# Kernel tuning notes

Measured on AMD Instinct MI355X. Metric: run time of the kernel, lower is better.

The kernel has to match this reference:

```python
import jax, jax.numpy as jnp
import numpy as np

B, S, D, U = 8, 2048, 256, 128


def setup_inputs() -> dict:
    key = jax.random.key(0)
    ks = jax.random.split(key, 5)
    inputs = jax.random.normal(ks[0], (B, S, D), dtype=jnp.float32)
    W_q = jax.random.normal(ks[1], (D, U), dtype=jnp.float32) * (1.0 / np.sqrt(D))
    W_k = jax.random.normal(ks[2], (D, U), dtype=jnp.float32) * (1.0 / np.sqrt(D))
    W_v = jax.random.normal(ks[3], (D, U), dtype=jnp.float32) * (1.0 / np.sqrt(D))
    W_o = jax.random.normal(ks[4], (U, D), dtype=jnp.float32) * (1.0 / np.sqrt(U))
    b_o = jnp.zeros((D,), dtype=jnp.float32)
    return {"inputs": inputs, "W_q": W_q, "W_k": W_k, "W_v": W_v, "W_o": W_o, "b_o": b_o}


def reference(inputs, W_q, W_k, W_v, W_o, b_o):
    # QKV projections: [B,S,D] @ [D,U] -> [B,S,U]
    Q = jnp.einsum('bsd,du->bsu', inputs, W_q)
    K = jnp.einsum('bsd,du->bsu', inputs, W_k)
    V = jnp.einsum('bsd,du->bsu', inputs, W_v)
    scale = 1.0 / jnp.sqrt(jnp.asarray(U, dtype=inputs.dtype))
    # scores: [B,S,S]
    attn = jnp.einsum('bqu,bku->bqk', Q, K) * scale
    w = jax.nn.softmax(attn, axis=-1)
    out = jnp.einsum('bqk,bku->bqu', w, V)  # [B,S,U]
    # output projection + residual
    return jnp.einsum('bsu,ud->bsd', out, W_o) + b_o + inputs
```

## Files before the change

kernel.cpp:

```cpp
#include <hip/hip_runtime.h>
#include <hip/hip_bf16.h>

#define B_ 8
#define S_ 2048
#define D_ 256
#define U_ 128
#define BS_ (B_*S_)

using bf16 = __hip_bfloat16;
typedef __attribute__((ext_vector_type(8))) __bf16 bf8v;
typedef __attribute__((ext_vector_type(4))) float f4v;
typedef __attribute__((ext_vector_type(16))) float f16v;
typedef __attribute__((ext_vector_type(4))) float float4v;
typedef __attribute__((ext_vector_type(4))) unsigned short us4;
typedef __attribute__((ext_vector_type(8))) unsigned short us8;
typedef __attribute__((ext_vector_type(4))) unsigned int u4v;
typedef __attribute__((ext_vector_type(2))) unsigned int u2v;

#define MFMA16(a,b,c) __builtin_amdgcn_mfma_f32_16x16x32_bf16((a),(b),(c),0,0,0)
#define MFMA32(a,b,c) __builtin_amdgcn_mfma_f32_32x32x16_bf16((a),(b),(c),0,0,0)

#if __has_builtin(__builtin_amdgcn_exp2f)
#define EXP2(x) __builtin_amdgcn_exp2f(x)
#else
#define EXP2(x) exp2f(x)
#endif

__device__ __forceinline__ unsigned short f2bits(float f){
  return __builtin_bit_cast(unsigned short, __float2bfloat16(f));
}
__device__ __forceinline__ float b2f(unsigned short u){
  return __builtin_bit_cast(float, ((unsigned)u) << 16);
}

__device__ __forceinline__ void plswap(unsigned &a, unsigned &b){
#if __has_builtin(__builtin_amdgcn_permlane32_swap)
  u2v r = __builtin_amdgcn_permlane32_swap(a, b, 0, 0);
  a = r[0]; b = r[1];
#else
  unsigned as = (unsigned)__shfl_xor((int)a, 32);
  unsigned bs = (unsigned)__shfl_xor((int)b, 32);
  bool hi = (threadIdx.x & 32) != 0;
  unsigned na = hi ? bs : a;
  unsigned nb = hi ? b  : as;
  a = na; b = nb;
#endif
}
__device__ __forceinline__ float cross_max(float x){
  unsigned a = __builtin_bit_cast(unsigned, x), b = a;
  plswap(a, b);
  return fmaxf(__builtin_bit_cast(float, a), __builtin_bit_cast(float, b));
}
__device__ __forceinline__ float cross_sum(float x){
  unsigned a = __builtin_bit_cast(unsigned, x), b = a;
  plswap(a, b);
  return __builtin_bit_cast(float, a) + __builtin_bit_cast(float, b);
}

__device__ __forceinline__ void gload16(const void* g, void* l){
  __builtin_amdgcn_global_load_lds(
    (const __attribute__((address_space(1))) char*)(unsigned long long)g,
    (__attribute__((address_space(3))) char*)(unsigned int)(unsigned long long)l,
    16, 0, 0);
}

__global__ __launch_bounds__(256) void prep_w_kernel(const float* __restrict__ Wq,
                                                     const float* __restrict__ Wk,
                                                     const float* __restrict__ Wv,
                                                     const float* __restrict__ Wo,
                                                     bf16* __restrict__ Wqf,
                                                     bf16* __restrict__ Wkf,
                                                     bf16* __restrict__ Wvf,
                                                     bf16* __restrict__ Wof){
  int t = blockIdx.x*256 + threadIdx.x;
  int which = t >> 12;
  int c = t & 4095;
  int lane = c & 63;
  int lq = lane & 15, g = lane >> 4;
  us8 v;
  if (which < 3){
    int nt = c >> 9;
    int ks = (c >> 6) & 7;
    const float* src = (which==0)?Wq:((which==1)?Wk:Wv);
    bf16* dst = (which==0)?Wqf:((which==1)?Wkf:Wvf);
    #pragma unroll
    for (int j=0;j<8;j++) v[j] = f2bits(src[(size_t)(ks*32 + g*8 + j)*U_ + nt*16 + lq]);
    *reinterpret_cast<us8*>(dst + (size_t)c*8) = v;
  } else {
    int nt = c >> 8;
    int ks = (c >> 6) & 3;
    #pragma unroll
    for (int j=0;j<8;j++) v[j] = f2bits(Wo[(size_t)(ks*32 + g*8 + j)*D_ + nt*16 + lq]);
    *reinterpret_cast<us8*>(Wof + (size_t)c*8) = v;
  }
}

__global__ __launch_bounds__(256) void qkv_kernel(const float* __restrict__ X,
                                                  const bf16* __restrict__ Wqf,
                                                  const bf16* __restrict__ Wkf,
                                                  const bf16* __restrict__ Wvf,
                                                  bf16* __restrict__ Q,
                                                  bf16* __restrict__ K,
                                                  bf16* __restrict__ Vt){
  __shared__ unsigned short Xls[32][264];

  const int tid  = threadIdx.x;
  const int w    = tid >> 6;
  const int lane = tid & 63;
  const int lq   = lane & 15;
  const int g    = lane >> 4;
  const int m0   = blockIdx.x*32;
  const int n0   = w*32;

  #pragma unroll
  for (int p=0; p<8; p++){
    int row = p*4 + (tid>>6);
    int col = (tid & 63)*4;
    float4v x = *reinterpret_cast<const float4v*>(X + (size_t)(m0+row)*D_ + col);
    us4 v;
    #pragma unroll
    for (int j=0;j<4;j++) v[j] = f2bits(x[j]);
    *reinterpret_cast<us4*>(&Xls[row][col]) = v;
  }
  __syncthreads();

  bf8v af[2][8];
  #pragma unroll
  for (int rt=0; rt<2; rt++)
    #pragma unroll
    for (int ks=0; ks<8; ks++)
      af[rt][ks] = *reinterpret_cast<const bf8v*>(&Xls[rt*16+lq][ks*32 + g*8]);

  #pragma unroll
  for (int which=0; which<3; which++){
    const bf16* Wf = (which==0) ? Wqf : ((which==1) ? Wkf : Wvf);
    f4v acc[2][2];
    #pragma unroll
    for (int rt=0;rt<2;rt++)
      #pragma unroll
      for (int ct=0;ct<2;ct++) acc[rt][ct] = (f4v){0.f,0.f,0.f,0.f};

    #pragma unroll
    for (int ks=0; ks<8; ks++){
      #pragma unroll
      for (int ct=0; ct<2; ct++){
        int nt = (n0>>4) + ct;
        bf8v b = *reinterpret_cast<const bf8v*>(Wf + ((size_t)((nt*8 + ks)*64 + lane) << 3));
        acc[0][ct] = MFMA16(af[0][ks], b, acc[0][ct]);
        acc[1][ct] = MFMA16(af[1][ks], b, acc[1][ct]);
      }
    }

    if (which==0){
      const float qscale = 0.12751745562008530f;
      #pragma unroll
      for (int rt=0;rt<2;rt++)
        #pragma unroll
        for (int ct=0;ct<2;ct++)
          #pragma unroll
          for (int r=0;r<4;r++)
            Q[(size_t)(m0+rt*16+g*4+r)*U_ + n0+ct*16+lq] = __float2bfloat16(acc[rt][ct][r]*qscale);
    } else if (which==1){
      #pragma unroll
      for (int rt=0;rt<2;rt++)
        #pragma unroll
        for (int ct=0;ct<2;ct++)
          #pragma unroll
          for (int r=0;r<4;r++)
            K[(size_t)(m0+rt*16+g*4+r)*U_ + n0+ct*16+lq] = __float2bfloat16(acc[rt][ct][r]);
    } else {
      #pragma unroll
      for (int rt=0;rt<2;rt++)
        #pragma unroll
        for (int ct=0;ct<2;ct++)
          #pragma unroll
          for (int r=0;r<4;r++){
            int m = m0 + rt*16 + g*4 + r;
            int bb = m >> 11;
            int ss = m & (S_-1);
            Vt[((size_t)bb*U_ + n0+ct*16+lq)*S_ + ss] = __float2bfloat16(acc[rt][ct][r]);
          }
    }
  }
}

__global__ __launch_bounds__(256) void flash_kernel(const bf16* __restrict__ Q,
                                                    const bf16* __restrict__ K,
                                                    const bf16* __restrict__ Vt,
                                                    bf16* __restrict__ Opart,
                                                    float* __restrict__ Mst,
                                                    float* __restrict__ Lst,
                                                    int nsplit){
  __shared__ bf16 Kls[2][64*128];
  __shared__ bf16 Vls[2][128*64];

  const int n    = blockIdx.x;
  const int b    = n & 7;
  const int m    = n >> 3;
  const int s    = m % nsplit;
  const int qt   = m / nsplit;
  const int w    = threadIdx.x >> 6;
  const int lane = threadIdx.x & 63;
  const int l5   = lane & 31;
  const int hi   = lane >> 5;
  const int q0   = qt*128 + w*32;

  const int NT = S_/64;
  const int t0 = (s*NT)/nsplit;
  const int t1 = ((s+1)*NT)/nsplit;

  const bf16* Qp = Q + (size_t)(b*S_ + q0 + l5)*U_ + hi*8;
  bf8v qf[8];
  #pragma unroll
  for (int uc=0; uc<8; uc++) qf[uc] = *reinterpret_cast<const bf8v*>(Qp + uc*16);

  f16v o[4];
  #pragma unroll
  for (int uc=0; uc<4; uc++)
    #pragma unroll
    for (int r=0; r<16; r++) o[uc][r] = 0.f;

  float mrow = -1e30f, lrow = 0.f;

  const bf16* Kbase = K  + (size_t)b*S_*U_;
  const bf16* Vtb   = Vt + (size_t)b*U_*S_;

  auto stageK = [&](int buf, int t){
    const int r0 = w*16;
    #pragma unroll
    for (int c=0; c<4; c++){
      int row  = r0 + c*4 + (lane>>4);
      int soff = ((lane&15)<<4) ^ ((row&7)<<4);
      const char* src = (const char*)(Kbase + (size_t)(t*64 + row)*U_) + soff;
      gload16(src, (void*)&Kls[buf][(r0 + c*4)*128]);
    }
  };
  auto stageV = [&](int buf, int t){
    const int r0 = w*32;
    #pragma unroll
    for (int c=0; c<4; c++){
      int u    = r0 + c*8 + (lane>>3);
      int soff = ((lane&7)<<4) ^ ((u&7)<<4);
      const char* src = (const char*)(Vtb + (size_t)u*S_ + t*64) + soff;
      gload16(src, (void*)&Vls[buf][(r0 + c*8)*64]);
    }
  };

  auto process = [&](f16v &st, const char* vb0, int sub){
    float p[16];
    #pragma unroll
    for (int r=0;r<16;r++) p[r] = st[r];

    float a0 = fmaxf(p[0],p[1]),  a1 = fmaxf(p[2],p[3]);
    float a2 = fmaxf(p[4],p[5]),  a3 = fmaxf(p[6],p[7]);
    float a4 = fmaxf(p[8],p[9]),  a5 = fmaxf(p[10],p[11]);
    float a6 = fmaxf(p[12],p[13]),a7 = fmaxf(p[14],p[15]);
    float b0 = fmaxf(a0,a1), b1 = fmaxf(a2,a3), b2 = fmaxf(a4,a5), b3 = fmaxf(a6,a7);
    float tm = fmaxf(fmaxf(b0,b1), fmaxf(b2,b3));
    tm = cross_max(tm);

    if (!__all(tm <= mrow + 11.54f)){
      float mn    = fmaxf(mrow, tm);
      float alpha = EXP2(mrow - mn);
      lrow *= alpha;
      #pragma unroll
      for (int uc=0;uc<4;uc++)
        #pragma unroll
        for (int r=0;r<16;r++) o[uc][r] *= alpha;
      mrow = mn;
    }

    #pragma unroll
    for (int r=0;r<16;r++) p[r] = EXP2(p[r]-mrow);
    float s0s = (p[0]+p[1]) + (p[2]+p[3]);
    float s1s = (p[4]+p[5]) + (p[6]+p[7]);
    float s2s = (p[8]+p[9]) + (p[10]+p[11]);
    float s3s = (p[12]+p[13]) + (p[14]+p[15]);
    lrow += cross_sum((s0s+s1s) + (s2s+s3s));

    unsigned c0 = (unsigned)f2bits(p[0])  | ((unsigned)f2bits(p[1])<<16);
    unsigned c1 = (unsigned)f2bits(p[2])  | ((unsigned)f2bits(p[3])<<16);
    unsigned c2 = (unsigned)f2bits(p[4])  | ((unsigned)f2bits(p[5])<<16);
    unsigned c3 = (unsigned)f2bits(p[6])  | ((unsigned)f2bits(p[7])<<16);
    unsigned c4 = (unsigned)f2bits(p[8])  | ((unsigned)f2bits(p[9])<<16);
    unsigned c5 = (unsigned)f2bits(p[10]) | ((unsigned)f2bits(p[11])<<16);
    unsigned c6 = (unsigned)f2bits(p[12]) | ((unsigned)f2bits(p[13])<<16);
    unsigned c7 = (unsigned)f2bits(p[14]) | ((unsigned)f2bits(p[15])<<16);
    plswap(c0, c2);
    plswap(c1, c3);
    plswap(c4, c6);
    plswap(c5, c7);
    u4v w0v = {c0, c1, c2, c3};
    u4v w1v = {c4, c5, c6, c7};
    bf8v pa0 = __builtin_bit_cast(bf8v, w0v);
    bf8v pa1 = __builtin_bit_cast(bf8v, w1v);

    __builtin_amdgcn_s_setprio(1);
    #pragma unroll
    for (int uc=0; uc<4; uc++){
      const char* vrow = vb0 + (uc*32 + l5)*128;
      bf8v v0 = *reinterpret_cast<const bf8v*>(vrow + ((sub*64      + hi*16) ^ ((l5&7)<<4)));
      bf8v v1 = *reinterpret_cast<const bf8v*>(vrow + ((sub*64 + 32 + hi*16) ^ ((l5&7)<<4)));
      o[uc] = MFMA32(v0, pa0, o[uc]);
      o[uc] = MFMA32(v1, pa1, o[uc]);
    }
    __builtin_amdgcn_s_setprio(0);
  };

  stageK(0, t0); stageV(0, t0);
  int cur = 0;
  for (int tt=t0; tt<t1; ++tt){
    int tn = (tt+1 < NT) ? (tt+1) : (NT-1);
    stageK(cur^1, tn); stageV(cur^1, tn);
    asm volatile("s_waitcnt vmcnt(8)" ::: "memory");
    __builtin_amdgcn_s_barrier();
    unsigned bufoff = (unsigned)cur * 16384u;
    asm volatile("" : "+v"(bufoff) : : "memory");
    const char* kb0 = (const char*)&Kls[0][0] + bufoff;
    const char* vb0 = (const char*)&Vls[0][0] + bufoff;

    f16v stA, stB;
    #pragma unroll
    for (int r=0;r<16;r++){ stA[r]=0.f; stB[r]=0.f; }
    __builtin_amdgcn_s_setprio(1);
    #pragma unroll
    for (int uc=0; uc<4; uc++){
      bf8v ka = *reinterpret_cast<const bf8v*>(kb0 + l5*256 + ((uc*64      + hi*16) ^ ((l5&7)<<4)));
      bf8v kc = *reinterpret_cast<const bf8v*>(kb0 + l5*256 + ((uc*64 + 32 + hi*16) ^ ((l5&7)<<4)));
      stA = MFMA32(ka, qf[2*uc],   stA);
      stA = MFMA32(kc, qf[2*uc+1], stA);
    }
    #pragma unroll
    for (int uc=0; uc<4; uc++){
      bf8v ka = *reinterpret_cast<const bf8v*>(kb0 + 8192 + l5*256 + ((uc*64      + hi*16) ^ ((l5&7)<<4)));
      bf8v kc = *reinterpret_cast<const bf8v*>(kb0 + 8192 + l5*256 + ((uc*64 + 32 + hi*16) ^ ((l5&7)<<4)));
      stB = MFMA32(ka, qf[2*uc],   stB);
      stB = MFMA32(kc, qf[2*uc+1], stB);
    }
    __builtin_amdgcn_s_setprio(0);

    process(stA, vb0, 0);
    process(stB, vb0, 1);

    asm volatile("" ::: "memory");
    __builtin_amdgcn_s_barrier();
    cur ^= 1;
  }

  const size_t rowg = (size_t)(b*S_ + q0 + l5);
  if (hi==0){
    Mst[(size_t)s*BS_ + rowg] = mrow;
    Lst[(size_t)s*BS_ + rowg] = lrow;
  }
  float inv = 1.0f / lrow;
  bf16* Op = Opart + (size_t)s*BS_*U_ + rowg*U_;
  #pragma unroll
  for (int uc=0; uc<4; uc++){
    #pragma unroll
    for (int g2=0; g2<4; g2++){
      us4 outv;
      #pragma unroll
      for (int j=0;j<4;j++) outv[j] = f2bits(o[uc][g2*4+j]*inv);
      *reinterpret_cast<us4*>(Op + uc*32 + g2*8 + hi*4) = outv;
    }
  }
}

template<int NS>
__global__ __launch_bounds__(256) void oproj_kernel(const bf16* __restrict__ Opart,
                                                    const float* __restrict__ Mst,
                                                    const float* __restrict__ Lst,
                                                    const bf16* __restrict__ Wof,
                                                    const float* __restrict__ X,
                                                    const float* __restrict__ bo,
                                                    float* __restrict__ Y){
  __shared__ unsigned short Als[64][136];

  const int tid  = threadIdx.x;
  const int w    = tid >> 6;
  const int lane = tid & 63;
  const int lq   = lane & 15;
  const int g    = lane >> 4;
  const int m0   = blockIdx.x*64;
  const int n0   = blockIdx.y*128;

  const unsigned short* Ou = reinterpret_cast<const unsigned short*>(Opart);
  #pragma unroll
  for (int p=0; p<4; p++){
    int rl  = p*16 + (tid>>4);
    int c8  = (tid & 15)*8;
    int row = m0 + rl;
    float cw[NS];
    float M = -1e30f;
    #pragma unroll
    for (int s=0;s<NS;s++){ cw[s] = Mst[(size_t)s*BS_ + row]; M = fmaxf(M, cw[s]); }
    float L = 0.f;
    #pragma unroll
    for (int s=0;s<NS;s++){ cw[s] = Lst[(size_t)s*BS_ + row]*EXP2(cw[s]-M); L += cw[s]; }
    float inv = 1.0f / L;
    float av[8];
    #pragma unroll
    for (int j=0;j<8;j++) av[j] = 0.f;
    #pragma unroll
    for (int s=0;s<NS;s++){
      us8 pp = *reinterpret_cast<const us8*>(Ou + (size_t)s*BS_*U_ + (size_t)row*U_ + c8);
      #pragma unroll
      for (int j=0;j<8;j++) av[j] += cw[s]*b2f(pp[j]);
    }
    us8 aw;
    #pragma unroll
    for (int j=0;j<8;j++) aw[j] = f2bits(av[j]*inv);
    *reinterpret_cast<us8*>(&Als[rl][c8]) = aw;
  }
  __syncthreads();

  f4v acc[8];
  #pragma unroll
  for (int i=0;i<8;i++) acc[i] = (f4v){0.f,0.f,0.f,0.f};

  #pragma unroll
  for (int ks=0; ks<4; ks++){
    bf8v a = *reinterpret_cast<const bf8v*>(&Als[w*16+lq][ks*32 + g*8]);
    #pragma unroll
    for (int nc=0;nc<8;nc++){
      int nt = (n0>>4) + nc;
      bf8v bb = *reinterpret_cast<const bf8v*>(Wof + ((size_t)((nt*4 + ks)*64 + lane) << 3));
      acc[nc] = MFMA16(a, bb, acc[nc]);
    }
  }

  #pragma unroll
  for (int nc=0;nc<8;nc++){
    int col = n0 + nc*16 + lq;
    float bias = bo[col];
    #pragma unroll
    for (int r=0;r<4;r++){
      int orow = m0 + w*16 + g*4 + r;
      Y[(size_t)orow*D_ + col] = acc[nc][r] + bias + X[(size_t)orow*D_ + col];
    }
  }
}

extern "C" void kernel_launch(void* const* d_in, const int* in_sizes, int n_in,
                              void* d_out, int out_size, void* d_ws, size_t ws_size,
                              hipStream_t stream) {
  (void)in_sizes; (void)n_in; (void)out_size;
  const float* X  = (const float*)d_in[0];
  const float* Wq = (const float*)d_in[1];
  const float* Wk = (const float*)d_in[2];
  const float* Wv = (const float*)d_in[3];
  const float* Wo = (const float*)d_in[4];
  const float* bo = (const float*)d_in[5];
  float* Y = (float*)d_out;

  const size_t MB = 1u<<20;
  int nsplit = (ws_size >= 30408704u) ? 4 : 2;

  char* ws = (char*)d_ws;
  bf16* Opart = (bf16*)ws;
  size_t off = (size_t)nsplit*4*MB;
  bf16* Qb  = (bf16*)(ws + off); off += 4*MB;
  bf16* Kb  = (bf16*)(ws + off); off += 4*MB;
  bf16* Vtb = (bf16*)(ws + off); off += 4*MB;
  bf16* Wqf = (bf16*)(ws + off); off += 65536;
  bf16* Wkf = (bf16*)(ws + off); off += 65536;
  bf16* Wvf = (bf16*)(ws + off); off += 65536;
  bf16* Wof = (bf16*)(ws + off); off += 65536;
  float* Mst = (float*)(ws + off); off += (size_t)nsplit*BS_*4;
  float* Lst = (float*)(ws + off);

  prep_w_kernel<<<dim3(64), dim3(256), 0, stream>>>(Wq, Wk, Wv, Wo, Wqf, Wkf, Wvf, Wof);
  qkv_kernel<<<dim3(BS_/32), dim3(256), 0, stream>>>(X, Wqf, Wkf, Wvf, Qb, Kb, Vtb);
  flash_kernel<<<dim3(16*nsplit*8), dim3(256), 0, stream>>>(Qb, Kb, Vtb, Opart, Mst, Lst, nsplit);
  if (nsplit == 4){
    oproj_kernel<4><<<dim3(BS_/64, 2), dim3(256), 0, stream>>>(Opart, Mst, Lst, Wof, X, bo, Y);
  } else {
    oproj_kernel<2><<<dim3(BS_/64, 2), dim3(256), 0, stream>>>(Opart, Mst, Lst, Wof, X, bo, Y);
  }
}
```

Before: 69.29 us.

## Halve flash KV tile to 32 keys, raise occupancy, allow 8-way split-K

The flash kernel now processes 32-key tiles instead of 64-key tiles. This halves LDS per block, drops the second score accumulator, and uses a new V swizzle for the narrower rows. Launch bounds now request 4 blocks per CU, and an 8-way KV split is used when the workspace is large enough, giving more blocks to fill the GPU. The cost is more loop iterations with barriers per key, and more partial outputs for the output-projection kernel to merge.

```diff
diff --git a/kernel.cpp b/kernel.cpp
--- a/kernel.cpp
+++ b/kernel.cpp
@@ -184,15 +184,15 @@
   }
 }
 
-__global__ __launch_bounds__(256) void flash_kernel(const bf16* __restrict__ Q,
-                                                    const bf16* __restrict__ K,
-                                                    const bf16* __restrict__ Vt,
-                                                    bf16* __restrict__ Opart,
-                                                    float* __restrict__ Mst,
-                                                    float* __restrict__ Lst,
-                                                    int nsplit){
-  __shared__ bf16 Kls[2][64*128];
-  __shared__ bf16 Vls[2][128*64];
+__global__ __launch_bounds__(256, 4) void flash_kernel(const bf16* __restrict__ Q,
+                                                       const bf16* __restrict__ K,
+                                                       const bf16* __restrict__ Vt,
+                                                       bf16* __restrict__ Opart,
+                                                       float* __restrict__ Mst,
+                                                       float* __restrict__ Lst,
+                                                       int nsplit){
+  __shared__ bf16 Kls[2][32*128];
+  __shared__ bf16 Vls[2][128*32];
 
   const int n    = blockIdx.x;
   const int b    = n & 7;
@@ -205,7 +205,7 @@
   const int hi   = lane >> 5;
   const int q0   = qt*128 + w*32;
 
-  const int NT = S_/64;
+  const int NT = S_/32;
   const int t0 = (s*NT)/nsplit;
   const int t1 = ((s+1)*NT)/nsplit;
 
@@ -226,31 +226,54 @@
   const bf16* Vtb   = Vt + (size_t)b*U_*S_;
 
   auto stageK = [&](int buf, int t){
-    const int r0 = w*16;
-    #pragma unroll
-    for (int c=0; c<4; c++){
+    const int r0 = w*8;
+    #pragma unroll
+    for (int c=0; c<2; c++){
       int row  = r0 + c*4 + (lane>>4);
       int soff = ((lane&15)<<4) ^ ((row&7)<<4);
-      const char* src = (const char*)(Kbase + (size_t)(t*64 + row)*U_) + soff;
+      const char* src = (const char*)(Kbase + (size_t)(t*32 + row)*U_) + soff;
       gload16(src, (void*)&Kls[buf][(r0 + c*4)*128]);
     }
   };
   auto stageV = [&](int buf, int t){
     const int r0 = w*32;
     #pragma unroll
-    for (int c=0; c<4; c++){
-      int u    = r0 + c*8 + (lane>>3);
-      int soff = ((lane&7)<<4) ^ ((u&7)<<4);
-      const char* src = (const char*)(Vtb + (size_t)u*S_ + t*64) + soff;
-      gload16(src, (void*)&Vls[buf][(r0 + c*8)*64]);
+    for (int c=0; c<2; c++){
+      int u    = r0 + c*16 + (lane>>2);
+      int soff = (((lane&3) ^ ((u>>1)&3)) << 4);
+      const char* src = (const char*)(Vtb + (size_t)u*S_ + t*32) + soff;
+      gload16(src, (void*)&Vls[buf][(r0 + c*16)*32]);
     }
   };
 
-  auto process = [&](f16v &st, const char* vb0, int sub){
+  stageK(0, t0); stageV(0, t0);
+  int cur = 0;
+  for (int tt=t0; tt<t1; ++tt){
+    int tn = (tt+1 < NT) ? (tt+1) : (NT-1);
+    stageK(cur^1, tn); stageV(cur^1, tn);
+    asm volatile("s_waitcnt vmcnt(4)" ::: "memory");
+    __builtin_amdgcn_s_barrier();
+    unsigned bufoff = (unsigned)cur * 8192u;
+    asm volatile("" : "+v"(bufoff) : : "memory");
+    const char* kb = (const char*)&Kls[0][0] + bufoff;
+    const char* vb = (const char*)&Vls[0][0] + bufoff;
+
+    f16v st;
+    #pragma unroll
+    for (int r=0;r<16;r++) st[r] = 0.f;
+    __builtin_amdgcn_s_setprio(1);
+    #pragma unroll
+    for (int uc=0; uc<4; uc++){
+      bf8v ka = *reinterpret_cast<const bf8v*>(kb + l5*256 + ((uc*64      + hi*16) ^ ((l5&7)<<4)));
+      bf8v kc = *reinterpret_cast<const bf8v*>(kb + l5*256 + ((uc*64 + 32 + hi*16) ^ ((l5&7)<<4)));
+      st = MFMA32(ka, qf[2*uc],   st);
+      st = MFMA32(kc, qf[2*uc+1], st);
+    }
+    __builtin_amdgcn_s_setprio(0);
+
     float p[16];
     #pragma unroll
     for (int r=0;r<16;r++) p[r] = st[r];
-
     float a0 = fmaxf(p[0],p[1]),  a1 = fmaxf(p[2],p[3]);
     float a2 = fmaxf(p[4],p[5]),  a3 = fmaxf(p[6],p[7]);
     float a4 = fmaxf(p[8],p[9]),  a5 = fmaxf(p[10],p[11]);
@@ -298,49 +321,15 @@
     __builtin_amdgcn_s_setprio(1);
     #pragma unroll
     for (int uc=0; uc<4; uc++){
-      const char* vrow = vb0 + (uc*32 + l5)*128;
-      bf8v v0 = *reinterpret_cast<const bf8v*>(vrow + ((sub*64      + hi*16) ^ ((l5&7)<<4)));
-      bf8v v1 = *reinterpret_cast<const bf8v*>(vrow + ((sub*64 + 32 + hi*16) ^ ((l5&7)<<4)));
+      int u = uc*32 + l5;
+      const char* vrow = vb + u*64;
+      int swz = ((u>>1)&3) << 4;
+      bf8v v0 = *reinterpret_cast<const bf8v*>(vrow + ((hi*16)      ^ swz));
+      bf8v v1 = *reinterpret_cast<const bf8v*>(vrow + ((32 + hi*16) ^ swz));
       o[uc] = MFMA32(v0, pa0, o[uc]);
       o[uc] = MFMA32(v1, pa1, o[uc]);
     }
     __builtin_amdgcn_s_setprio(0);
-  };
-
-  stageK(0, t0); stageV(0, t0);
-  int cur = 0;
-  for (int tt=t0; tt<t1; ++tt){
-    int tn = (tt+1 < NT) ? (tt+1) : (NT-1);
-    stageK(cur^1, tn); stageV(cur^1, tn);
-    asm volatile("s_waitcnt vmcnt(8)" ::: "memory");
-    __builtin_amdgcn_s_barrier();
-    unsigned bufoff = (unsigned)cur * 16384u;
-    asm volatile("" : "+v"(bufoff) : : "memory");
-    const char* kb0 = (const char*)&Kls[0][0] + bufoff;
-    const char* vb0 = (const char*)&Vls[0][0] + bufoff;
-
-    f16v stA, stB;
-    #pragma unroll
-    for (int r=0;r<16;r++){ stA[r]=0.f; stB[r]=0.f; }
-    __builtin_amdgcn_s_setprio(1);
-    #pragma unroll
-    for (int uc=0; uc<4; uc++){
-      bf8v ka = *reinterpret_cast<const bf8v*>(kb0 + l5*256 + ((uc*64      + hi*16) ^ ((l5&7)<<4)));
-      bf8v kc = *reinterpret_cast<const bf8v*>(kb0 + l5*256 + ((uc*64 + 32 + hi*16) ^ ((l5&7)<<4)));
-      stA = MFMA32(ka, qf[2*uc],   stA);
-      stA = MFMA32(kc, qf[2*uc+1], stA);
-    }
-    #pragma unroll
-    for (int uc=0; uc<4; uc++){
-      bf8v ka = *reinterpret_cast<const bf8v*>(kb0 + 8192 + l5*256 + ((uc*64      + hi*16) ^ ((l5&7)<<4)));
-      bf8v kc = *reinterpret_cast<const bf8v*>(kb0 + 8192 + l5*256 + ((uc*64 + 32 + hi*16) ^ ((l5&7)<<4)));
-      stB = MFMA32(ka, qf[2*uc],   stB);
-      stB = MFMA32(kc, qf[2*uc+1], stB);
-    }
-    __builtin_amdgcn_s_setprio(0);
-
-    process(stA, vb0, 0);
-    process(stB, vb0, 1);
 
     asm volatile("" ::: "memory");
     __builtin_amdgcn_s_barrier();
@@ -454,7 +443,7 @@
   float* Y = (float*)d_out;
 
   const size_t MB = 1u<<20;
-  int nsplit = (ws_size >= 30408704u) ? 4 : 2;
+  int nsplit = (ws_size >= 47448064u) ? 8 : ((ws_size >= 30408704u) ? 4 : 2);
 
   char* ws = (char*)d_ws;
   bf16* Opart = (bf16*)ws;
@@ -472,7 +461,9 @@
   prep_w_kernel<<<dim3(64), dim3(256), 0, stream>>>(Wq, Wk, Wv, Wo, Wqf, Wkf, Wvf, Wof);
   qkv_kernel<<<dim3(BS_/32), dim3(256), 0, stream>>>(X, Wqf, Wkf, Wvf, Qb, Kb, Vtb);
   flash_kernel<<<dim3(16*nsplit*8), dim3(256), 0, stream>>>(Qb, Kb, Vtb, Opart, Mst, Lst, nsplit);
-  if (nsplit == 4){
+  if (nsplit == 8){
+    oproj_kernel<8><<<dim3(BS_/64, 2), dim3(256), 0, stream>>>(Opart, Mst, Lst, Wof, X, bo, Y);
+  } else if (nsplit == 4){
     oproj_kernel<4><<<dim3(BS_/64, 2), dim3(256), 0, stream>>>(Opart, Mst, Lst, Wof, X, bo, Y);
   } else {
     oproj_kernel<2><<<dim3(BS_/64, 2), dim3(256), 0, stream>>>(Opart, Mst, Lst, Wof, X, bo, Y);
```

After: 91.89 us. 1.33x slower.
